# Optimization experiments

Measured on AMD Instinct MI355X. Metric: run time of the kernel, lower is better.

Reference implementation:

```python
import jax, jax.numpy as jnp
import numpy as np

N, D, H = 8192, 256, 128
KEEP_RATIO = 0.5
TEMP = 1.0
COS_EPS = 1e-4  # torch CosineSimilarity eps
NEG = -9e15


def setup_inputs() -> dict:
    key = jax.random.key(0)
    k1, k2, k3, k4 = jax.random.split(key, 4)
    features = jax.random.normal(k1, (N, D), dtype=jnp.float32)
    adj = jax.random.randint(k2, (N, N), 0, 2, dtype=jnp.int32)
    # module init: Linear weights ~ N(0, 0.001)
    Wq = jax.random.normal(k3, (H, D), dtype=jnp.float32) * 0.001
    Wk = jax.random.normal(k4, (H, D), dtype=jnp.float32) * 0.001
    return {"features": features, "adj": adj, "Wq": Wq, "Wk": Wk}


def _cos_normalize(x):
    # torch cosine: x / max(||x||, eps)
    n = jnp.linalg.norm(x, axis=-1, keepdims=True)
    return x / jnp.maximum(n, COS_EPS)


def reference(features, adj, Wq, Wk):
    # projections [N, H]
    Qn = _cos_normalize(features @ Wq.T)
    Kn = _cos_normalize(features @ Wk.T)
    # raw_att[i, j] = cos(Wq f_j, Wk f_i)  -> [N, N]
    raw_att = Kn @ Qn.T
    att = jnp.where(adj > 0, raw_att, NEG) * TEMP
    att = jax.nn.softmax(att, axis=1)
    prop_fea = att @ features  # [N, D]
    # nodes with no neighbors keep their own features
    adj_mask = (jnp.sum(adj, axis=1) > 0).astype(features.dtype)[:, None]
    prop_fea = adj_mask * prop_fea + (1.0 - adj_mask) * features
    # gate=None branch: fixed keep_ratio mixing
    return (1.0 - KEEP_RATIO) * prop_fea + KEEP_RATIO * features
```

## Files before the change

kernel.cpp:

```cpp
#include <hip/hip_runtime.h>
#include <stdint.h>
#include <stddef.h>

#define NN 8192
#define DD 256
#define HH 128

typedef short bf16x8 __attribute__((ext_vector_type(8)));
typedef float f32x4  __attribute__((ext_vector_type(4)));
typedef int   i32x4  __attribute__((ext_vector_type(4)));

static __device__ __forceinline__ short f2bf(float x){
  unsigned u = __float_as_uint(x);
  u = (u + 0x7FFFu + ((u >> 16) & 1u)) >> 16;
  return (short)(unsigned short)u;
}

static __device__ __forceinline__ bf16x8 cvt8(const float* p){
  f32x4 a = *(const f32x4*)p;
  f32x4 b = *(const f32x4*)(p + 4);
  bf16x8 o;
  o[0]=f2bf(a[0]); o[1]=f2bf(a[1]); o[2]=f2bf(a[2]); o[3]=f2bf(a[3]);
  o[4]=f2bf(b[0]); o[5]=f2bf(b[1]); o[6]=f2bf(b[2]); o[7]=f2bf(b[3]);
  return o;
}

static __device__ __forceinline__ bf16x8 ld16(const void* p){
  i32x4 v = *(const i32x4*)p;
  return __builtin_bit_cast(bf16x8, v);
}

__global__ __launch_bounds__(256) void k_transpose(const float* __restrict__ f,
                                                   unsigned short* __restrict__ ft){
  __shared__ unsigned short tile[64][65];
  int t  = threadIdx.x;
  int i0 = blockIdx.x * 64, d0 = blockIdx.y * 64;
  int r0 = t >> 6, c = t & 63;
  for (int it = 0; it < 16; ++it){
    int r = r0 + it * 4;
    tile[c][r] = (unsigned short)f2bf(f[(size_t)(i0 + r) * DD + d0 + c]);
  }
  __syncthreads();
  for (int it = 0; it < 16; ++it){
    int rr = r0 + it * 4;
    ft[(size_t)(d0 + rr) * NN + i0 + c] = tile[rr][c];
  }
}

__global__ __launch_bounds__(256) void k_proj(const float* __restrict__ f,
                                              const float* __restrict__ Wq,
                                              const float* __restrict__ Wk,
                                              unsigned short* __restrict__ Qn,
                                              unsigned short* __restrict__ Kn){
  int t = threadIdx.x, wave = t >> 6, l = t & 63;
  int i0 = blockIdx.x * 64 + wave * 16;
  int lr = l & 15, lk = l >> 4;
  bf16x8 ka[8];
  for (int ks = 0; ks < 8; ++ks)
    ka[ks] = cvt8(f + (size_t)(i0 + lr) * DD + ks * 32 + lk * 8);
  for (int pj = 0; pj < 2; ++pj){
    const float* W = pj ? Wk : Wq;
    unsigned short* out = pj ? Kn : Qn;
    f32x4 acc[8];
    for (int n = 0; n < 8; ++n) acc[n] = (f32x4){0.f,0.f,0.f,0.f};
    for (int ks = 0; ks < 8; ++ks)
      for (int n = 0; n < 8; ++n){
        bf16x8 bb = cvt8(W + (size_t)(n * 16 + lr) * DD + ks * 32 + lk * 8);
        acc[n] = __builtin_amdgcn_mfma_f32_16x16x32_bf16(ka[ks], bb, acc[n], 0, 0, 0);
      }
    for (int r = 0; r < 4; ++r){
      float n2 = 0.f;
      for (int n = 0; n < 8; ++n){ float v = acc[n][r]; n2 += v * v; }
      n2 += __shfl_xor(n2, 1); n2 += __shfl_xor(n2, 2);
      n2 += __shfl_xor(n2, 4); n2 += __shfl_xor(n2, 8);
      float s = 1.f / fmaxf(sqrtf(n2), 1e-4f);
      int row = i0 + lk * 4 + r;
      for (int n = 0; n < 8; ++n)
        out[(size_t)row * HH + n * 16 + lr] = (unsigned short)f2bf(acc[n][r] * s);
    }
  }
}

__global__ __launch_bounds__(256, 2) void k_attn(const int* __restrict__ adj,
      const unsigned short* __restrict__ Qn, const unsigned short* __restrict__ Kn,
      const unsigned short* __restrict__ ft,
      float* __restrict__ num_p, float* __restrict__ den_p){
  __shared__ __align__(16) char smem[57344];
  char* qn_s = smem;
  char* ft_s = smem + 16384;
  char* w_s  = smem + 49152;
  int t = threadIdx.x, wave = t >> 6, l = t & 63;
  int ib = blockIdx.x >> 2, js = blockIdx.x & 3;
  int i0 = ib * 64;
  int jbase = js * 2048;
  int lr = l & 15, lk = l >> 4;
  int swz = (l & 7) << 4;
  bf16x8 ka[4];
  {
    const unsigned short* kp = Kn + (size_t)(i0 + wave * 16 + lr) * HH;
    for (int ks = 0; ks < 4; ++ks) ka[ks] = ld16(kp + ks * 32 + lk * 8);
  }
  f32x4 pv[2][8];
  for (int a = 0; a < 2; ++a) for (int b = 0; b < 8; ++b) pv[a][b] = (f32x4){0.f,0.f,0.f,0.f};
  float dacc[4] = {0.f, 0.f, 0.f, 0.f};
  int rgp = wave & 1, dh = wave >> 1;
  int qrow = t >> 4, qc = t & 15;
  int frow = t >> 3, fc = t & 7;

  for (int step = 0; step < 32; ++step){
    int j0 = jbase + step * 64;
    __syncthreads();
    for (int it = 0; it < 4; ++it){
      int r = qrow + it * 16;
      i32x4 v = *(const i32x4*)(Qn + (size_t)(j0 + r) * HH + qc * 8);
      *(i32x4*)(qn_s + r * 256 + ((qc * 16) ^ ((r & 7) << 4))) = v;
    }
    for (int it = 0; it < 8; ++it){
      int d2 = frow + it * 32;
      i32x4 v = *(const i32x4*)(ft + (size_t)d2 * NN + j0 + fc * 8);
      *(i32x4*)(ft_s + d2 * 128 + ((fc * 16) ^ ((d2 & 7) << 4))) = v;
    }
    int adjv[4][4];
    for (int r = 0; r < 4; ++r){
      const int* ap = adj + (size_t)(i0 + wave * 16 + lk * 4 + r) * NN + j0 + lr;
      for (int cg = 0; cg < 4; ++cg)
        adjv[cg][r] = __builtin_nontemporal_load(ap + cg * 16);
    }
    __syncthreads();
    f32x4 sa[4];
    for (int cg = 0; cg < 4; ++cg) sa[cg] = (f32x4){0.f,0.f,0.f,0.f};
    for (int ks = 0; ks < 4; ++ks){
      int kb = (ks * 64 + lk * 16) ^ swz;
      for (int cg = 0; cg < 4; ++cg){
        bf16x8 bq = ld16(qn_s + (cg * 16 + lr) * 256 + kb);
        sa[cg] = __builtin_amdgcn_mfma_f32_16x16x32_bf16(ka[ks], bq, sa[cg], 0, 0, 0);
      }
    }
    for (int cg = 0; cg < 4; ++cg)
      for (int r = 0; r < 4; ++r){
        float w = adjv[cg][r] > 0 ? __expf(sa[cg][r]) : 0.f;
        dacc[r] += w;
        int row = wave * 16 + lk * 4 + r;
        *(unsigned short*)(w_s + row * 128 + ((cg * 32 + lr * 2) ^ ((row & 7) << 4)))
            = (unsigned short)f2bf(w);
      }
    __syncthreads();
    for (int ks = 0; ks < 2; ++ks){
      int kb = (ks * 64 + lk * 16) ^ swz;
      bf16x8 a0 = ld16(w_s + (rgp * 32 + lr) * 128 + kb);
      bf16x8 a1 = ld16(w_s + (rgp * 32 + 16 + lr) * 128 + kb);
      for (int dn = 0; dn < 8; ++dn){
        int dl = dh * 128 + dn * 16 + lr;
        bf16x8 bv = ld16(ft_s + dl * 128 + kb);
        pv[0][dn] = __builtin_amdgcn_mfma_f32_16x16x32_bf16(a0, bv, pv[0][dn], 0, 0, 0);
        pv[1][dn] = __builtin_amdgcn_mfma_f32_16x16x32_bf16(a1, bv, pv[1][dn], 0, 0, 0);
      }
    }
  }
  for (int r = 0; r < 4; ++r){
    float v = dacc[r];
    v += __shfl_xor(v, 1); v += __shfl_xor(v, 2);
    v += __shfl_xor(v, 4); v += __shfl_xor(v, 8);
    if (lr == 0) den_p[(size_t)js * NN + i0 + wave * 16 + lk * 4 + r] = v;
  }
  float* np = num_p + (size_t)js * NN * DD;
  for (int rgi = 0; rgi < 2; ++rgi)
    for (int dn = 0; dn < 8; ++dn)
      for (int r = 0; r < 4; ++r){
        int row = i0 + rgp * 32 + rgi * 16 + lk * 4 + r;
        int col = dh * 128 + dn * 16 + lr;
        np[(size_t)row * DD + col] = pv[rgi][dn][r];
      }
}

__global__ __launch_bounds__(256) void k_final(const float* __restrict__ num_p,
                                               const float* __restrict__ den_p,
                                               const float* __restrict__ f,
                                               float* __restrict__ out){
  int gid = blockIdx.x * 256 + threadIdx.x;
  int i = gid >> 6;
  f32x4 nv = (f32x4){0.f,0.f,0.f,0.f};
  float dv = 0.f;
  for (int s = 0; s < 4; ++s){
    nv += *(const f32x4*)(num_p + (size_t)s * NN * DD + (size_t)gid * 4);
    dv += den_p[(size_t)s * NN + i];
  }
  f32x4 fv = *(const f32x4*)(f + (size_t)gid * 4);
  f32x4 o;
  if (dv > 0.f){
    float inv = 0.5f / dv;
    o = nv * inv + fv * 0.5f;
  } else {
    o = fv;
  }
  *(f32x4*)(out + (size_t)gid * 4) = o;
}

extern "C" void kernel_launch(void* const* d_in, const int* in_sizes, int n_in,
                              void* d_out, int out_size, void* d_ws, size_t ws_size,
                              hipStream_t stream){
  (void)in_sizes; (void)n_in; (void)out_size;
  const float* feat = (const float*)d_in[0];
  const int*   adj  = (const int*)d_in[1];
  const float* Wq   = (const float*)d_in[2];
  const float* Wk   = (const float*)d_in[3];
  float* out = (float*)d_out;
  char* ws = (char*)d_ws;
  unsigned short* Qn = (unsigned short*)(ws);
  unsigned short* Kn = (unsigned short*)(ws + (2u << 20));
  unsigned short* ft = (unsigned short*)(ws + (4u << 20));
  float* num_p = (float*)(ws + (8u << 20));
  float* den_p = (float*)(ws + (40u << 20));
  if (ws_size < (40u << 20) + (4u * NN * 4u)) return;

  k_transpose<<<dim3(128, 4), 256, 0, stream>>>(feat, ft);
  k_proj<<<128, 256, 0, stream>>>(feat, Wq, Wk, Qn, Kn);
  k_attn<<<512, 256, 0, stream>>>(adj, Qn, Kn, ft, num_p, den_p);
  k_final<<<2048, 256, 0, stream>>>(num_p, den_p, feat, out);
}
```

Before: 233.0 us.

## Bit-pack adjacency and restructure attention with 32x32 MFMA and async LDS staging

Adds a pre-pass that packs the int32 adjacency into a bitmask with wave ballots, so the attention kernel reads 1 bit per entry instead of 4 bytes. The attention kernel is rewritten to use 32x32x16 MFMA tiles, to read Q straight from global memory, and to keep the exp weights in registers, moving them between lanes with packed bf16 converts and cross-half shuffles instead of an LDS round trip. Feature tiles are staged with global_load_lds into a swizzled layout that the transpose kernel now writes, and the two j-halves of each block are reduced through LDS at the end. The cost is an extra full pass over adj in the pack kernel, plus higher register and LDS use.

```diff
diff --git a/kernel.cpp b/kernel.cpp
--- a/kernel.cpp
+++ b/kernel.cpp
@@ -6,16 +6,16 @@
 #define DD 256
 #define HH 128
 
-typedef short bf16x8 __attribute__((ext_vector_type(8)));
-typedef float f32x4  __attribute__((ext_vector_type(4)));
-typedef int   i32x4  __attribute__((ext_vector_type(4)));
+typedef short bf16x8  __attribute__((ext_vector_type(8)));
+typedef float f32x4   __attribute__((ext_vector_type(4)));
+typedef float f32x16  __attribute__((ext_vector_type(16)));
+typedef int   i32x4   __attribute__((ext_vector_type(4)));
 
 static __device__ __forceinline__ short f2bf(float x){
   unsigned u = __float_as_uint(x);
   u = (u + 0x7FFFu + ((u >> 16) & 1u)) >> 16;
   return (short)(unsigned short)u;
 }
-
 static __device__ __forceinline__ bf16x8 cvt8(const float* p){
   f32x4 a = *(const f32x4*)p;
   f32x4 b = *(const f32x4*)(p + 4);
@@ -24,10 +24,22 @@
   o[4]=f2bf(b[0]); o[5]=f2bf(b[1]); o[6]=f2bf(b[2]); o[7]=f2bf(b[3]);
   return o;
 }
-
 static __device__ __forceinline__ bf16x8 ld16(const void* p){
   i32x4 v = *(const i32x4*)p;
   return __builtin_bit_cast(bf16x8, v);
+}
+static __device__ __forceinline__ unsigned cvtpk(float lo, float hi){
+  unsigned r;
+  asm("v_cvt_pk_bf16_f32 %0, %1, %2" : "=v"(r) : "v"(lo), "v"(hi));
+  return r;
+}
+static __device__ __forceinline__ bf16x8 mk8(unsigned a, unsigned b, unsigned c, unsigned d){
+  i32x4 t; t[0]=(int)a; t[1]=(int)b; t[2]=(int)c; t[3]=(int)d;
+  return __builtin_bit_cast(bf16x8, t);
+}
+static __device__ __forceinline__ void gl_lds16(const void* g, void* l){
+  __builtin_amdgcn_global_load_lds((const __attribute__((address_space(1))) void*)g,
+                                   (__attribute__((address_space(3))) void*)l, 16, 0, 0);
 }
 
 __global__ __launch_bounds__(256) void k_transpose(const float* __restrict__ f,
@@ -41,9 +53,12 @@
     tile[c][r] = (unsigned short)f2bf(f[(size_t)(i0 + r) * DD + d0 + c]);
   }
   __syncthreads();
+  int jlog = i0 + c;
   for (int it = 0; it < 16; ++it){
     int rr = r0 + it * 4;
-    ft[(size_t)(d0 + rr) * NN + i0 + c] = tile[rr][c];
+    int d  = d0 + rr;
+    int jp = (jlog & ~127) | ((((jlog >> 3) ^ d) & 15) << 3) | (jlog & 7);
+    ft[(size_t)d * NN + jp] = tile[rr][c];
   }
 }
 
@@ -81,96 +96,145 @@
   }
 }
 
-__global__ __launch_bounds__(256, 2) void k_attn(const int* __restrict__ adj,
+__global__ __launch_bounds__(256) void k_pack(const int* __restrict__ adj,
+                                              unsigned* __restrict__ bits){
+  int wave = threadIdx.x >> 6, l = threadIdx.x & 63;
+  int gw   = blockIdx.x * 4 + wave;
+  int row  = gw >> 1, half = gw & 1;
+  const int* ap = adj + (size_t)row * NN + half * 4096 + l;
+  unsigned long long* bp =
+      (unsigned long long*)(bits + (size_t)row * 256 + half * 128);
+  for (int c = 0; c < 64; ++c){
+    int v = __builtin_nontemporal_load(ap + c * 64);
+    unsigned long long m = __ballot(v > 0);
+    if (l == 0) bp[c] = m;
+  }
+}
+
+__global__ __launch_bounds__(256, 2) void k_attn(
+      const unsigned* __restrict__ bits,
       const unsigned short* __restrict__ Qn, const unsigned short* __restrict__ Kn,
       const unsigned short* __restrict__ ft,
       float* __restrict__ num_p, float* __restrict__ den_p){
-  __shared__ __align__(16) char smem[57344];
-  char* qn_s = smem;
-  char* ft_s = smem + 16384;
-  char* w_s  = smem + 49152;
+  __shared__ __attribute__((aligned(256))) char smem[65792];
   int t = threadIdx.x, wave = t >> 6, l = t & 63;
+  int ig = wave >> 1, jg = wave & 1;
+  int lc = l & 31, h = l >> 5;
   int ib = blockIdx.x >> 2, js = blockIdx.x & 3;
   int i0 = ib * 64;
   int jbase = js * 2048;
-  int lr = l & 15, lk = l >> 4;
-  int swz = (l & 7) << 4;
-  bf16x8 ka[4];
+  int irow = i0 + ig * 32 + lc;
+
+  bf16x8 kb[8];
   {
-    const unsigned short* kp = Kn + (size_t)(i0 + wave * 16 + lr) * HH;
-    for (int ks = 0; ks < 4; ++ks) ka[ks] = ld16(kp + ks * 32 + lk * 8);
-  }
-  f32x4 pv[2][8];
-  for (int a = 0; a < 2; ++a) for (int b = 0; b < 8; ++b) pv[a][b] = (f32x4){0.f,0.f,0.f,0.f};
-  float dacc[4] = {0.f, 0.f, 0.f, 0.f};
-  int rgp = wave & 1, dh = wave >> 1;
-  int qrow = t >> 4, qc = t & 15;
-  int frow = t >> 3, fc = t & 7;
-
-  for (int step = 0; step < 32; ++step){
-    int j0 = jbase + step * 64;
+    const unsigned short* kp = Kn + (size_t)irow * HH + h * 8;
+    #pragma unroll
+    for (int hs = 0; hs < 8; ++hs) kb[hs] = ld16(kp + hs * 16);
+  }
+  f32x16 pv[8];
+  #pragma unroll
+  for (int dt = 0; dt < 8; ++dt)
+    #pragma unroll
+    for (int e = 0; e < 16; ++e) pv[dt][e] = 0.f;
+  float dacc = 0.f;
+
+  auto stage = [&](int j0){
+    #pragma unroll
+    for (int q = 0; q < 16; ++q){
+      int d = q * 16 + wave * 4 + (l >> 4);
+      const unsigned short* src = ft + (size_t)d * NN + j0 + (l & 15) * 8;
+      gl_lds16(src, smem + q * 4096 + wave * 1024);
+    }
+  };
+
+  stage(jbase);
+  for (int s = 0; s < 16; ++s){
+    int j0 = jbase + s * 128;
+    int jw = j0 + jg * 64;
+    unsigned bw0 = bits[(size_t)irow * 256 + (jw >> 5)];
+    unsigned bw1 = bits[(size_t)irow * 256 + (jw >> 5) + 1];
+
+    f32x16 st[2];
+    #pragma unroll
+    for (int jt = 0; jt < 2; ++jt)
+      #pragma unroll
+      for (int e = 0; e < 16; ++e) st[jt][e] = 0.f;
+    #pragma unroll
+    for (int jt = 0; jt < 2; ++jt){
+      const unsigned short* qp = Qn + (size_t)(jw + jt * 32 + lc) * HH + h * 8;
+      #pragma unroll
+      for (int hs = 0; hs < 8; ++hs)
+        st[jt] = __builtin_amdgcn_mfma_f32_32x32x16_bf16(ld16(qp + hs * 16), kb[hs], st[jt], 0, 0, 0);
+    }
+
+    bf16x8 pa[2][2];
+    #pragma unroll
+    for (int jt = 0; jt < 2; ++jt){
+      unsigned bw = jt ? bw1 : bw0;
+      float w[16];
+      #pragma unroll
+      for (int r = 0; r < 16; ++r){
+        int jp = (r & 3) + 8 * (r >> 2) + 4 * h;
+        float wv = ((bw >> jp) & 1u) ? __expf(st[jt][r]) : 0.f;
+        w[r] = wv; dacc += wv;
+      }
+      unsigned x0 = cvtpk(w[0],  w[1]),  x1 = cvtpk(w[2],  w[3]);
+      unsigned x2 = cvtpk(w[4],  w[5]),  x3 = cvtpk(w[6],  w[7]);
+      unsigned x4 = cvtpk(w[8],  w[9]),  x5 = cvtpk(w[10], w[11]);
+      unsigned x6 = cvtpk(w[12], w[13]), x7 = cvtpk(w[14], w[15]);
+      unsigned za = __shfl_xor(h ? x0 : x2, 32);
+      unsigned zb = __shfl_xor(h ? x1 : x3, 32);
+      unsigned zc = __shfl_xor(h ? x4 : x6, 32);
+      unsigned zd = __shfl_xor(h ? x5 : x7, 32);
+      pa[jt][0] = h ? mk8(za, zb, x2, x3) : mk8(x0, x1, za, zb);
+      pa[jt][1] = h ? mk8(zc, zd, x6, x7) : mk8(x4, x5, zc, zd);
+    }
+
     __syncthreads();
-    for (int it = 0; it < 4; ++it){
-      int r = qrow + it * 16;
-      i32x4 v = *(const i32x4*)(Qn + (size_t)(j0 + r) * HH + qc * 8);
-      *(i32x4*)(qn_s + r * 256 + ((qc * 16) ^ ((r & 7) << 4))) = v;
-    }
-    for (int it = 0; it < 8; ++it){
-      int d2 = frow + it * 32;
-      i32x4 v = *(const i32x4*)(ft + (size_t)d2 * NN + j0 + fc * 8);
-      *(i32x4*)(ft_s + d2 * 128 + ((fc * 16) ^ ((d2 & 7) << 4))) = v;
-    }
-    int adjv[4][4];
-    for (int r = 0; r < 4; ++r){
-      const int* ap = adj + (size_t)(i0 + wave * 16 + lk * 4 + r) * NN + j0 + lr;
-      for (int cg = 0; cg < 4; ++cg)
-        adjv[cg][r] = __builtin_nontemporal_load(ap + cg * 16);
-    }
-    __syncthreads();
-    f32x4 sa[4];
-    for (int cg = 0; cg < 4; ++cg) sa[cg] = (f32x4){0.f,0.f,0.f,0.f};
+    #pragma unroll
     for (int ks = 0; ks < 4; ++ks){
-      int kb = (ks * 64 + lk * 16) ^ swz;
-      for (int cg = 0; cg < 4; ++cg){
-        bf16x8 bq = ld16(qn_s + (cg * 16 + lr) * 256 + kb);
-        sa[cg] = __builtin_amdgcn_mfma_f32_16x16x32_bf16(ka[ks], bq, sa[cg], 0, 0, 0);
-      }
-    }
-    for (int cg = 0; cg < 4; ++cg)
-      for (int r = 0; r < 4; ++r){
-        float w = adjv[cg][r] > 0 ? __expf(sa[cg][r]) : 0.f;
-        dacc[r] += w;
-        int row = wave * 16 + lk * 4 + r;
-        *(unsigned short*)(w_s + row * 128 + ((cg * 32 + lr * 2) ^ ((row & 7) << 4)))
-            = (unsigned short)f2bf(w);
-      }
-    __syncthreads();
-    for (int ks = 0; ks < 2; ++ks){
-      int kb = (ks * 64 + lk * 16) ^ swz;
-      bf16x8 a0 = ld16(w_s + (rgp * 32 + lr) * 128 + kb);
-      bf16x8 a1 = ld16(w_s + (rgp * 32 + 16 + lr) * 128 + kb);
-      for (int dn = 0; dn < 8; ++dn){
-        int dl = dh * 128 + dn * 16 + lr;
-        bf16x8 bv = ld16(ft_s + dl * 128 + kb);
-        pv[0][dn] = __builtin_amdgcn_mfma_f32_16x16x32_bf16(a0, bv, pv[0][dn], 0, 0, 0);
-        pv[1][dn] = __builtin_amdgcn_mfma_f32_16x16x32_bf16(a1, bv, pv[1][dn], 0, 0, 0);
-      }
-    }
-  }
-  for (int r = 0; r < 4; ++r){
-    float v = dacc[r];
-    v += __shfl_xor(v, 1); v += __shfl_xor(v, 2);
-    v += __shfl_xor(v, 4); v += __shfl_xor(v, 8);
-    if (lr == 0) den_p[(size_t)js * NN + i0 + wave * 16 + lk * 4 + r] = v;
-  }
-  float* np = num_p + (size_t)js * NN * DD;
-  for (int rgi = 0; rgi < 2; ++rgi)
-    for (int dn = 0; dn < 8; ++dn)
-      for (int r = 0; r < 4; ++r){
-        int row = i0 + rgp * 32 + rgi * 16 + lk * 4 + r;
-        int col = dh * 128 + dn * 16 + lr;
-        np[(size_t)row * DD + col] = pv[rgi][dn][r];
-      }
+      bf16x8 a = pa[ks >> 1][ks & 1];
+      int up = ((jg * 8 + ks * 2 + h) ^ (lc & 15)) << 4;
+      #pragma unroll
+      for (int dt = 0; dt < 8; ++dt){
+        int d = dt * 32 + lc;
+        bf16x8 b = ld16(smem + d * 256 + up);
+        pv[dt] = __builtin_amdgcn_mfma_f32_32x32x16_bf16(a, b, pv[dt], 0, 0, 0);
+      }
+    }
+    if (s < 15){
+      __syncthreads();
+      stage(j0 + 128);
+    }
+  }
+
+  float dsum = dacc + __shfl_xor(dacc, 32);
+  __syncthreads();
+  float* red  = (float*)smem;
+  float* dred = (float*)(smem + 65536);
+  if (jg == 0){
+    #pragma unroll
+    for (int dt = 0; dt < 8; ++dt)
+      #pragma unroll
+      for (int r = 0; r < 16; ++r){
+        int ip = (r & 3) + 8 * (r >> 2) + 4 * h;
+        red[ig * 8192 + ip * 256 + dt * 32 + lc] = pv[dt][r];
+      }
+    if (h == 0) dred[ig * 32 + lc] = dsum;
+  }
+  __syncthreads();
+  if (jg == 1){
+    float* np = num_p + (size_t)js * NN * DD;
+    #pragma unroll
+    for (int dt = 0; dt < 8; ++dt)
+      #pragma unroll
+      for (int r = 0; r < 16; ++r){
+        int ip = (r & 3) + 8 * (r >> 2) + 4 * h;
+        float v = pv[dt][r] + red[ig * 8192 + ip * 256 + dt * 32 + lc];
+        np[(size_t)(i0 + ig * 32 + ip) * DD + dt * 32 + lc] = v;
+      }
+    if (h == 0) den_p[(size_t)js * NN + i0 + ig * 32 + lc] = dsum + dred[ig * 32 + lc];
+  }
 }
 
 __global__ __launch_bounds__(256) void k_final(const float* __restrict__ num_p,
@@ -181,6 +245,7 @@
   int i = gid >> 6;
   f32x4 nv = (f32x4){0.f,0.f,0.f,0.f};
   float dv = 0.f;
+  #pragma unroll
   for (int s = 0; s < 4; ++s){
     nv += *(const f32x4*)(num_p + (size_t)s * NN * DD + (size_t)gid * 4);
     dv += den_p[(size_t)s * NN + i];
@@ -206,15 +271,17 @@
   const float* Wk   = (const float*)d_in[3];
   float* out = (float*)d_out;
   char* ws = (char*)d_ws;
-  unsigned short* Qn = (unsigned short*)(ws);
-  unsigned short* Kn = (unsigned short*)(ws + (2u << 20));
-  unsigned short* ft = (unsigned short*)(ws + (4u << 20));
-  float* num_p = (float*)(ws + (8u << 20));
-  float* den_p = (float*)(ws + (40u << 20));
-  if (ws_size < (40u << 20) + (4u * NN * 4u)) return;
+  unsigned short* Qn   = (unsigned short*)(ws);
+  unsigned short* Kn   = (unsigned short*)(ws + (2u << 20));
+  unsigned short* ft   = (unsigned short*)(ws + (4u << 20));
+  unsigned*       bits = (unsigned*)(ws + (8u << 20));
+  float*          num_p = (float*)(ws + (16u << 20));
+  float*          den_p = (float*)(ws + (48u << 20));
+  if (ws_size < (48u << 20) + 131072u) return;
 
   k_transpose<<<dim3(128, 4), 256, 0, stream>>>(feat, ft);
   k_proj<<<128, 256, 0, stream>>>(feat, Wq, Wk, Qn, Kn);
-  k_attn<<<512, 256, 0, stream>>>(adj, Qn, Kn, ft, num_p, den_p);
+  k_pack<<<4096, 256, 0, stream>>>(adj, bits);
+  k_attn<<<512, 256, 0, stream>>>(bits, Qn, Kn, ft, num_p, den_p);
   k_final<<<2048, 256, 0, stream>>>(num_p, den_p, feat, out);
 }
```

New measurement: 320.2 us. 1.37x slower.
